# Kernel tuning notes

Hardware: AMD Instinct MI355X
Metric: run time of the kernel (lower is better)

The kernel has to match this reference:

```python
import jax, jax.numpy as jnp
import numpy as np

GAMMA = 0.2
P = 3
N = 16384


def setup_inputs() -> dict:
    key = jax.random.key(0)
    k1, k2 = jax.random.split(key)
    y_pred = jax.random.normal(k1, (N, 2), dtype=jnp.float32)
    y_true = jax.random.randint(k2, (N,), 0, 2, dtype=jnp.int32)
    return {"y_pred": y_pred, "y_true": y_true}


def reference(y_pred, y_true):
    # softmax over classes, take probability of class 1 -> [N]
    s = jax.nn.softmax(y_pred, axis=-1)[:, 1]
    pos_mask = (y_true == 1)
    neg_mask = ~pos_mask
    # difference[j, i] = pos_i - neg_j - gamma  (rows: negatives, cols: positives)
    diff = s[None, :] - s[:, None] - GAMMA  # [N, N]
    pair = neg_mask[:, None] & pos_mask[None, :]
    valid = pair & (diff < 0.0)
    # sum of (-diff)^p over masked entries == hinge^p penalty
    contrib = jnp.where(valid, (-diff) ** P, jnp.zeros_like(diff))
    return jnp.sum(contrib)
```

## Files before the change

### kernel.cpp

```cpp
#include <hip/hip_runtime.h>
#include <math.h>

#define GAMMA_F 0.2f
#define NT 1024
#define NPART 16

__device__ __forceinline__ float sigmoid_from_logits(float y0, float y1) {
    return 1.0f / (1.0f + __expf(y0 - y1));
}

__global__ __launch_bounds__(NT) void fused_pair_kernel(
        const float* __restrict__ y_pred, const int* __restrict__ y_true,
        int n, float* __restrict__ out) {
    __shared__ float row_a[NT + 4];
    __shared__ float col_s[NT + 4];
    __shared__ int cnts[2];
    __shared__ float wsum[NT / 64];

    int tid = threadIdx.x;
    int lane = tid & 63;
    unsigned long long lt = (1ULL << lane) - 1ULL;
    if (tid < 2) cnts[tid] = 0;
    __syncthreads();

    {
        int i = blockIdx.x * NT + tid;
        bool in = (i < n);
        float a = 0.0f;
        bool is_pos = false;
        if (in) {
            float2 y = ((const float2*)y_pred)[i];
            a = sigmoid_from_logits(y.x, y.y) - GAMMA_F;
            is_pos = (y_true[i] == 1);
        }
        unsigned long long m = __ballot(is_pos);
        int base = 0;
        if (lane == 0) base = atomicAdd(&cnts[0], __popcll(m));
        base = __shfl(base, 0, 64);
        if (is_pos) row_a[base + __popcll(m & lt)] = a;
    }
    {
        int j = blockIdx.y * NT + tid;
        bool in = (j < n);
        float s = 0.0f;
        bool is_neg = false;
        if (in) {
            float2 y = ((const float2*)y_pred)[j];
            s = sigmoid_from_logits(y.x, y.y);
            is_neg = (y_true[j] != 1);
        }
        unsigned long long m = __ballot(is_neg);
        int base = 0;
        if (lane == 0) base = atomicAdd(&cnts[1], __popcll(m));
        base = __shfl(base, 0, 64);
        if (is_neg) col_s[base + __popcll(m & lt)] = s;
    }
    __syncthreads();

    int n_rows = cnts[0];
    int n_cols = cnts[1];
    if (tid < 4) {
        row_a[n_rows + tid] = 1e30f;
        col_s[n_cols + tid] = -1e30f;
    }
    __syncthreads();

    int p = tid & (NPART - 1);
    int g = tid >> 4;
    int nf4 = (n_cols + 3) >> 2;
    const float4* col4 = (const float4*)col_s;

    float acc0 = 0.0f, acc1 = 0.0f, acc2 = 0.0f, acc3 = 0.0f;
    for (int r = g * 4; r < n_rows; r += (NT / NPART) * 4) {
        float a0 = row_a[r + 0];
        float a1 = row_a[r + 1];
        float a2 = row_a[r + 2];
        float a3 = row_a[r + 3];
        for (int k = p; k < nf4; k += NPART) {
            float4 b = col4[k];
            float t;
            t = fmaxf(b.x - a0, 0.0f); acc0 += (t * t) * t;
            t = fmaxf(b.x - a1, 0.0f); acc1 += (t * t) * t;
            t = fmaxf(b.x - a2, 0.0f); acc2 += (t * t) * t;
            t = fmaxf(b.x - a3, 0.0f); acc3 += (t * t) * t;
            t = fmaxf(b.y - a0, 0.0f); acc0 += (t * t) * t;
            t = fmaxf(b.y - a1, 0.0f); acc1 += (t * t) * t;
            t = fmaxf(b.y - a2, 0.0f); acc2 += (t * t) * t;
            t = fmaxf(b.y - a3, 0.0f); acc3 += (t * t) * t;
            t = fmaxf(b.z - a0, 0.0f); acc0 += (t * t) * t;
            t = fmaxf(b.z - a1, 0.0f); acc1 += (t * t) * t;
            t = fmaxf(b.z - a2, 0.0f); acc2 += (t * t) * t;
            t = fmaxf(b.z - a3, 0.0f); acc3 += (t * t) * t;
            t = fmaxf(b.w - a0, 0.0f); acc0 += (t * t) * t;
            t = fmaxf(b.w - a1, 0.0f); acc1 += (t * t) * t;
            t = fmaxf(b.w - a2, 0.0f); acc2 += (t * t) * t;
            t = fmaxf(b.w - a3, 0.0f); acc3 += (t * t) * t;
        }
    }
    float acc = (acc0 + acc1) + (acc2 + acc3);

    #pragma unroll
    for (int off = 32; off > 0; off >>= 1) acc += __shfl_down(acc, off, 64);
    int wave = tid >> 6;
    if (lane == 0) wsum[wave] = acc;
    __syncthreads();
    if (tid == 0) {
        float s = 0.0f;
        #pragma unroll
        for (int w = 0; w < NT / 64; ++w) s += wsum[w];
        atomicAdd(out, s);
    }
}

extern "C" void kernel_launch(void* const* d_in, const int* in_sizes, int n_in,
                              void* d_out, int out_size, void* d_ws, size_t ws_size,
                              hipStream_t stream) {
    const float* y_pred = (const float*)d_in[0];
    const int* y_true = (const int*)d_in[1];
    int n = in_sizes[1];
    float* out = (float*)d_out;
    (void)d_ws; (void)ws_size;

    int g = (n + NT - 1) / NT;
    dim3 grid(g, g), block(NT);
    fused_pair_kernel<<<grid, block, 0, stream>>>(y_pred, y_true, n, out);
}
```

Baseline: 64.21 us.

## Replace all-pairs hinge sum with bucketed power-sum prefix moments in one block

Swaps the O(N^2) tiled pairwise loop for a single-block algorithm. The kernel builds a histogram of negative scores over fixed buckets, counting-sorts the negatives into shared memory, and computes suffix sums of the count, sum, sum of squares and sum of cubes per bucket in double precision. Each positive then expands (b-a)^3 over the bucket suffix in closed form and handles only its own bucket by direct pairwise terms. This removes the quadratic compute and the grid-wide atomics. In exchange it runs on a single workgroup, caps stored negatives at a fixed shared-memory capacity, and relies on fixed bucket bounds.

```diff
diff --git a/kernel.cpp b/kernel.cpp
--- a/kernel.cpp
+++ b/kernel.cpp
@@ -3,112 +3,189 @@
 
 #define GAMMA_F 0.2f
 #define NT 1024
-#define NPART 16
-
-__device__ __forceinline__ float sigmoid_from_logits(float y0, float y1) {
-    return 1.0f / (1.0f + __expf(y0 - y1));
-}
-
-__global__ __launch_bounds__(NT) void fused_pair_kernel(
+#define NB 1024
+#define CAP 9920
+#define DLO 0.25f
+#define DSCALE (NB / 1.5f)
+
+__device__ __forceinline__ float sig2(float2 y) {
+    return 1.0f / (1.0f + __expf(y.x - y.y));
+}
+
+__device__ __forceinline__ int bucket_of(float x) {
+    int k = (int)floorf((x + DLO) * DSCALE);
+    return k < 0 ? 0 : (k >= NB ? NB - 1 : k);
+}
+
+extern "C" __global__ __launch_bounds__(NT) void softauc_bucket_kernel(
         const float* __restrict__ y_pred, const int* __restrict__ y_true,
         int n, float* __restrict__ out) {
-    __shared__ float row_a[NT + 4];
-    __shared__ float col_s[NT + 4];
-    __shared__ int cnts[2];
-    __shared__ float wsum[NT / 64];
-
+    __shared__ int cnt[NB];
+    __shared__ int cur[NB];
+    __shared__ float negv[CAP];
+    __shared__ float4 ssum[NB];
+    __shared__ int wscan[NT / 64];
+    __shared__ double4 wtot[NT / 64];
+    __shared__ double wred[NT / 64];
+
+    const float2* __restrict__ yp2 = (const float2*)y_pred;
     int tid = threadIdx.x;
     int lane = tid & 63;
-    unsigned long long lt = (1ULL << lane) - 1ULL;
-    if (tid < 2) cnts[tid] = 0;
+    int wave = tid >> 6;
+
+    cnt[tid] = 0;
+    __syncthreads();
+
+    const int stride4 = NT * 4;
+    int nfull = n - (n % stride4);
+
+    for (int base = 0; base < nfull; base += stride4) {
+        float2 ya = yp2[base + tid];
+        float2 yb = yp2[base + NT + tid];
+        float2 yc = yp2[base + 2 * NT + tid];
+        float2 yd = yp2[base + 3 * NT + tid];
+        int ta = y_true[base + tid];
+        int tb = y_true[base + NT + tid];
+        int tc = y_true[base + 2 * NT + tid];
+        int td = y_true[base + 3 * NT + tid];
+        if (ta != 1) atomicAdd(&cnt[bucket_of(sig2(ya))], 1);
+        if (tb != 1) atomicAdd(&cnt[bucket_of(sig2(yb))], 1);
+        if (tc != 1) atomicAdd(&cnt[bucket_of(sig2(yc))], 1);
+        if (td != 1) atomicAdd(&cnt[bucket_of(sig2(yd))], 1);
+    }
+    for (int r = nfull + tid; r < n; r += NT) {
+        if (y_true[r] != 1) atomicAdd(&cnt[bucket_of(sig2(yp2[r]))], 1);
+    }
     __syncthreads();
 
     {
-        int i = blockIdx.x * NT + tid;
-        bool in = (i < n);
-        float a = 0.0f;
-        bool is_pos = false;
-        if (in) {
-            float2 y = ((const float2*)y_pred)[i];
-            a = sigmoid_from_logits(y.x, y.y) - GAMMA_F;
-            is_pos = (y_true[i] == 1);
-        }
-        unsigned long long m = __ballot(is_pos);
-        int base = 0;
-        if (lane == 0) base = atomicAdd(&cnts[0], __popcll(m));
-        base = __shfl(base, 0, 64);
-        if (is_pos) row_a[base + __popcll(m & lt)] = a;
-    }
+        int v = cnt[tid];
+        int inc = v;
+        #pragma unroll
+        for (int d = 1; d < 64; d <<= 1) {
+            int t = __shfl_up(inc, d, 64);
+            if (lane >= d) inc += t;
+        }
+        if (lane == 63) wscan[wave] = inc;
+        __syncthreads();
+        int off = 0;
+        for (int w = 0; w < wave; ++w) off += wscan[w];
+        cur[tid] = off + inc - v;
+    }
+    __syncthreads();
+
+    for (int base = 0; base < nfull; base += stride4) {
+        float2 ya = yp2[base + tid];
+        float2 yb = yp2[base + NT + tid];
+        float2 yc = yp2[base + 2 * NT + tid];
+        float2 yd = yp2[base + 3 * NT + tid];
+        int ta = y_true[base + tid];
+        int tb = y_true[base + NT + tid];
+        int tc = y_true[base + 2 * NT + tid];
+        int td = y_true[base + 3 * NT + tid];
+        if (ta != 1) { float b = sig2(ya); int p = atomicAdd(&cur[bucket_of(b)], 1); if (p < CAP) negv[p] = b; }
+        if (tb != 1) { float b = sig2(yb); int p = atomicAdd(&cur[bucket_of(b)], 1); if (p < CAP) negv[p] = b; }
+        if (tc != 1) { float b = sig2(yc); int p = atomicAdd(&cur[bucket_of(b)], 1); if (p < CAP) negv[p] = b; }
+        if (td != 1) { float b = sig2(yd); int p = atomicAdd(&cur[bucket_of(b)], 1); if (p < CAP) negv[p] = b; }
+    }
+    for (int r = nfull + tid; r < n; r += NT) {
+        if (y_true[r] != 1) { float b = sig2(yp2[r]); int p = atomicAdd(&cur[bucket_of(b)], 1); if (p < CAP) negv[p] = b; }
+    }
+    __syncthreads();
+
     {
-        int j = blockIdx.y * NT + tid;
-        bool in = (j < n);
-        float s = 0.0f;
-        bool is_neg = false;
-        if (in) {
-            float2 y = ((const float2*)y_pred)[j];
-            s = sigmoid_from_logits(y.x, y.y);
-            is_neg = (y_true[j] != 1);
-        }
-        unsigned long long m = __ballot(is_neg);
-        int base = 0;
-        if (lane == 0) base = atomicAdd(&cnts[1], __popcll(m));
-        base = __shfl(base, 0, 64);
-        if (is_neg) col_s[base + __popcll(m & lt)] = s;
-    }
-    __syncthreads();
-
-    int n_rows = cnts[0];
-    int n_cols = cnts[1];
-    if (tid < 4) {
-        row_a[n_rows + tid] = 1e30f;
-        col_s[n_cols + tid] = -1e30f;
-    }
-    __syncthreads();
-
-    int p = tid & (NPART - 1);
-    int g = tid >> 4;
-    int nf4 = (n_cols + 3) >> 2;
-    const float4* col4 = (const float4*)col_s;
-
-    float acc0 = 0.0f, acc1 = 0.0f, acc2 = 0.0f, acc3 = 0.0f;
-    for (int r = g * 4; r < n_rows; r += (NT / NPART) * 4) {
-        float a0 = row_a[r + 0];
-        float a1 = row_a[r + 1];
-        float a2 = row_a[r + 2];
-        float a3 = row_a[r + 3];
-        for (int k = p; k < nf4; k += NPART) {
-            float4 b = col4[k];
-            float t;
-            t = fmaxf(b.x - a0, 0.0f); acc0 += (t * t) * t;
-            t = fmaxf(b.x - a1, 0.0f); acc1 += (t * t) * t;
-            t = fmaxf(b.x - a2, 0.0f); acc2 += (t * t) * t;
-            t = fmaxf(b.x - a3, 0.0f); acc3 += (t * t) * t;
-            t = fmaxf(b.y - a0, 0.0f); acc0 += (t * t) * t;
-            t = fmaxf(b.y - a1, 0.0f); acc1 += (t * t) * t;
-            t = fmaxf(b.y - a2, 0.0f); acc2 += (t * t) * t;
-            t = fmaxf(b.y - a3, 0.0f); acc3 += (t * t) * t;
-            t = fmaxf(b.z - a0, 0.0f); acc0 += (t * t) * t;
-            t = fmaxf(b.z - a1, 0.0f); acc1 += (t * t) * t;
-            t = fmaxf(b.z - a2, 0.0f); acc2 += (t * t) * t;
-            t = fmaxf(b.z - a3, 0.0f); acc3 += (t * t) * t;
-            t = fmaxf(b.w - a0, 0.0f); acc0 += (t * t) * t;
-            t = fmaxf(b.w - a1, 0.0f); acc1 += (t * t) * t;
-            t = fmaxf(b.w - a2, 0.0f); acc2 += (t * t) * t;
-            t = fmaxf(b.w - a3, 0.0f); acc3 += (t * t) * t;
-        }
-    }
-    float acc = (acc0 + acc1) + (acc2 + acc3);
+        int k = (NB - 1) - tid;
+        int e = min(cur[k], CAP);
+        int b0 = max(e - cnt[k], 0);
+        double c0 = (double)cnt[k], c1 = 0.0, c2 = 0.0, c3 = 0.0;
+        for (int i = b0; i < e; ++i) {
+            double b = (double)negv[i];
+            double b2 = b * b;
+            c1 += b; c2 += b2; c3 += b2 * b;
+        }
+        double i0 = c0, i1 = c1, i2 = c2, i3 = c3;
+        #pragma unroll
+        for (int d = 1; d < 64; d <<= 1) {
+            double t0 = __shfl_up(i0, d, 64);
+            double t1 = __shfl_up(i1, d, 64);
+            double t2 = __shfl_up(i2, d, 64);
+            double t3 = __shfl_up(i3, d, 64);
+            if (lane >= d) { i0 += t0; i1 += t1; i2 += t2; i3 += t3; }
+        }
+        if (lane == 63) wtot[wave] = make_double4(i0, i1, i2, i3);
+        __syncthreads();
+        double o0 = 0.0, o1 = 0.0, o2 = 0.0, o3 = 0.0;
+        for (int w = 0; w < wave; ++w) {
+            double4 t = wtot[w];
+            o0 += t.x; o1 += t.y; o2 += t.z; o3 += t.w;
+        }
+        ssum[k] = make_float4((float)(o0 + i0 - c0), (float)(o1 + i1 - c1),
+                              (float)(o2 + i2 - c2), (float)(o3 + i3 - c3));
+    }
+    __syncthreads();
+
+    double acc = 0.0;
+    for (int base = 0; base < nfull; base += stride4) {
+        float2 ya = yp2[base + tid];
+        float2 yb = yp2[base + NT + tid];
+        float2 yc = yp2[base + 2 * NT + tid];
+        float2 yd = yp2[base + 3 * NT + tid];
+        int ta = y_true[base + tid];
+        int tb = y_true[base + NT + tid];
+        int tc = y_true[base + 2 * NT + tid];
+        int td = y_true[base + 3 * NT + tid];
+        #pragma unroll
+        for (int q = 0; q < 4; ++q) {
+            int t = (q == 0) ? ta : (q == 1) ? tb : (q == 2) ? tc : td;
+            if (t == 1) {
+                float2 y = (q == 0) ? ya : (q == 1) ? yb : (q == 2) ? yc : yd;
+                float a = sig2(y) - GAMMA_F;
+                int ka = bucket_of(a);
+                float4 ss = ssum[ka];
+                double ad = (double)a;
+                acc += (double)ss.w - 3.0 * ad * (double)ss.z
+                     + 3.0 * ad * ad * (double)ss.y - ad * ad * ad * (double)ss.x;
+                int e = min(cur[ka], CAP);
+                int b0 = max(e - cnt[ka], 0);
+                for (int i = b0; i < e; ++i) {
+                    float b = negv[i];
+                    if (b > a) {
+                        double tt = (double)b - ad;
+                        acc += tt * tt * tt;
+                    }
+                }
+            }
+        }
+    }
+    for (int r = nfull + tid; r < n; r += NT) {
+        if (y_true[r] == 1) {
+            float a = sig2(yp2[r]) - GAMMA_F;
+            int ka = bucket_of(a);
+            float4 ss = ssum[ka];
+            double ad = (double)a;
+            acc += (double)ss.w - 3.0 * ad * (double)ss.z
+                 + 3.0 * ad * ad * (double)ss.y - ad * ad * ad * (double)ss.x;
+            int e = min(cur[ka], CAP);
+            int b0 = max(e - cnt[ka], 0);
+            for (int i = b0; i < e; ++i) {
+                float b = negv[i];
+                if (b > a) {
+                    double tt = (double)b - ad;
+                    acc += tt * tt * tt;
+                }
+            }
+        }
+    }
 
     #pragma unroll
     for (int off = 32; off > 0; off >>= 1) acc += __shfl_down(acc, off, 64);
-    int wave = tid >> 6;
-    if (lane == 0) wsum[wave] = acc;
+    if (lane == 0) wred[wave] = acc;
     __syncthreads();
     if (tid == 0) {
-        float s = 0.0f;
-        #pragma unroll
-        for (int w = 0; w < NT / 64; ++w) s += wsum[w];
-        atomicAdd(out, s);
+        double t = 0.0;
+        #pragma unroll
+        for (int w = 0; w < NT / 64; ++w) t += wred[w];
+        out[0] = (float)t;
     }
 }
 
@@ -119,9 +196,8 @@
     const int* y_true = (const int*)d_in[1];
     int n = in_sizes[1];
     float* out = (float*)d_out;
-    (void)d_ws; (void)ws_size;
-
-    int g = (n + NT - 1) / NT;
-    dim3 grid(g, g), block(NT);
-    fused_pair_kernel<<<grid, block, 0, stream>>>(y_pred, y_true, n, out);
-}
+    (void)d_ws; (void)ws_size; (void)n_in; (void)out_size;
+
+    dim3 grid(1), block(NT);
+    softauc_bucket_kernel<<<grid, block, 0, stream>>>(y_pred, y_true, n, out);
+}
```

Result: slower. 98.95 us (+54.1%).
